# Kernel optimization log

Measured on AMD Instinct MI355X. Metric: run time of the kernel, lower is better.

## Reference

```python
import jax, jax.numpy as jnp
import numpy as np

B, H, S, D = 2, 16, 2048, 64

def setup_inputs() -> dict:
    key = jax.random.key(0)
    kq, kk, kv = jax.random.split(key, 3)
    Q = jax.random.normal(kq, (B, H, S, D), dtype=jnp.float32)
    K = jax.random.normal(kk, (B, H, S, D), dtype=jnp.float32)
    V = jax.random.normal(kv, (B, H, S, D), dtype=jnp.float32)
    d_sqrt = jnp.float32(np.sqrt(D))  # 8.0
    return {"Q": Q, "K": K, "V": V, "d_sqrt": d_sqrt}

def reference(Q, K, V, d_sqrt):
    # scores = Q @ K^T / d_sqrt  -> softmax over last axis -> @ V
    scores = jnp.einsum("bhqd,bhkd->bhqk", Q, K) / d_sqrt  # [B,H,S,S]
    attention = jax.nn.softmax(scores, axis=-1)
    return jnp.einsum("bhqk,bhkd->bhqd", attention, V)
```

## Files before the change

kernel.cpp:

```cpp
#include <hip/hip_runtime.h>
#include <hip/hip_bf16.h>


#define S_LEN 2048
#define DHEAD 64
#define QB 128
#define KB 64
#define NT (S_LEN / KB)
#define LDK 72

typedef __attribute__((ext_vector_type(8))) short short8;
typedef __attribute__((ext_vector_type(4))) short short4v;
typedef __attribute__((ext_vector_type(4))) float f32x4;

__device__ __forceinline__ unsigned pk2(float a, float b) {
  unsigned r;
  asm("v_cvt_pk_bf16_f32 %0, %1, %2" : "=v"(r) : "v"(a), "v"(b));
  return r;
}

#if __has_builtin(__builtin_amdgcn_exp2f)
#define EXP2(x) __builtin_amdgcn_exp2f(x)
#else
__device__ __forceinline__ float exp2_asm(float x) {
  float r; asm("v_exp_f32 %0, %1" : "=v"(r) : "v"(x)); return r;
}
#define EXP2(x) exp2_asm(x)
#endif

__device__ __forceinline__ f32x4 mfma16(short4v a, short4v b, f32x4 c) {
#if __has_builtin(__builtin_amdgcn_mfma_f32_16x16x16bf16_1k)
  return __builtin_amdgcn_mfma_f32_16x16x16bf16_1k(a, b, c, 0, 0, 0);
#else
  asm volatile("s_nop 1\n\t"
               "v_mfma_f32_16x16x16_bf16 %0, %1, %2, %0\n\t"
               "s_nop 7"
               : "+v"(c) : "v"(a), "v"(b));
  return c;
#endif
}

union frag8 { short8 s; unsigned u[4]; };
union frag4 { short4v s4; unsigned u[2]; };
union vpair { short8 s8; short4v h[2]; };

__global__ __launch_bounds__(512, 4) void attn_fwd_kernel(
    const float* __restrict__ Q, const float* __restrict__ K,
    const float* __restrict__ V, const float* __restrict__ dscale,
    float* __restrict__ O) {
  const int bx = blockIdx.x;
  const int qt = bx & 15;
  const int bh = bx >> 4;
  const float scale = 1.4426950408889634f / dscale[0];

  __shared__ unsigned short Klds[2][KB][LDK];
  __shared__ unsigned short Vtlds[2][DHEAD][LDK];

  const int tid = threadIdx.x;
  const int wid = tid >> 6;
  const int lane = tid & 63;
  const int lhi = lane >> 4;
  const int llo = lane & 15;

  const float* Qb = Q + (size_t)bh * S_LEN * DHEAD;
  const float* Kb = K + (size_t)bh * S_LEN * DHEAD;
  const float* Vb = V + (size_t)bh * S_LEN * DHEAD;
  float* Ob = O + (size_t)bh * S_LEN * DHEAD;

  frag8 qf0, qf1;
  {
    const int qrow = qt * QB + wid * 16 + llo;
    const float* qp = Qb + (size_t)qrow * DHEAD + lhi * 8;
    float4 a = *(const float4*)(qp);
    float4 b = *(const float4*)(qp + 4);
    float4 c = *(const float4*)(qp + 32);
    float4 d = *(const float4*)(qp + 36);
    qf0.u[0] = pk2(a.x * scale, a.y * scale);
    qf0.u[1] = pk2(a.z * scale, a.w * scale);
    qf0.u[2] = pk2(b.x * scale, b.y * scale);
    qf0.u[3] = pk2(b.z * scale, b.w * scale);
    qf1.u[0] = pk2(c.x * scale, c.y * scale);
    qf1.u[1] = pk2(c.z * scale, c.w * scale);
    qf1.u[2] = pk2(d.x * scale, d.y * scale);
    qf1.u[3] = pk2(d.z * scale, d.w * scale);
  }

  frag4 ones;
  ones.u[0] = 0x3f803f80u;
  ones.u[1] = 0x3f803f80u;

  f32x4 o[4], ol;
#pragma unroll
  for (int t = 0; t < 4; ++t) o[t] = (f32x4)0.0f;
  ol = (f32x4)0.0f;

  const int kr = tid >> 3;
  const int kc = (tid & 7) * 8;
  const int vd = tid & 63;
  const int vg0 = (wid >> 2) * 32 + (wid & 3) * 4;

  float4 ka, kb2;
  float va[8];
  {
    const float* kp = Kb + (size_t)(0 * KB + kr) * DHEAD + kc;
    ka = *(const float4*)kp;
    kb2 = *(const float4*)(kp + 4);
    const float* vp0 = Vb + (size_t)(0 * KB + vg0) * DHEAD + vd;
#pragma unroll
    for (int j = 0; j < 4; ++j) va[j] = vp0[j * DHEAD];
#pragma unroll
    for (int j = 0; j < 4; ++j) va[4 + j] = vp0[(16 + j) * DHEAD];
  }

  for (int kt = 0; kt < NT; ++kt) {
    const int cb = kt & 1;
    {
      uint4 kw;
      kw.x = pk2(ka.x, ka.y); kw.y = pk2(ka.z, ka.w);
      kw.z = pk2(kb2.x, kb2.y); kw.w = pk2(kb2.z, kb2.w);
      *(uint4*)&Klds[cb][kr][kc] = kw;
      uint4 vw;
      vw.x = pk2(va[0], va[1]); vw.y = pk2(va[2], va[3]);
      vw.z = pk2(va[4], va[5]); vw.w = pk2(va[6], va[7]);
      *(uint4*)&Vtlds[cb][vd][wid * 8] = vw;
    }
    __syncthreads();

    {
      const int nk = (kt + 1 < NT) ? kt + 1 : 0;
      const float* kp = Kb + (size_t)(nk * KB + kr) * DHEAD + kc;
      ka = *(const float4*)kp;
      kb2 = *(const float4*)(kp + 4);
      const float* vp0 = Vb + (size_t)(nk * KB + vg0) * DHEAD + vd;
#pragma unroll
      for (int j = 0; j < 4; ++j) va[j] = vp0[j * DHEAD];
#pragma unroll
      for (int j = 0; j < 4; ++j) va[4 + j] = vp0[(16 + j) * DHEAD];
    }

    f32x4 s[4];
    __builtin_amdgcn_s_setprio(1);
#pragma unroll
    for (int t = 0; t < 4; ++t) {
      short8 kf0 = *(const short8*)&Klds[cb][t * 16 + llo][lhi * 8];
      short8 kf1 = *(const short8*)&Klds[cb][t * 16 + llo][32 + lhi * 8];
      f32x4 acc = (f32x4)0.0f;
      acc = __builtin_amdgcn_mfma_f32_16x16x32_bf16(kf0, qf0.s, acc, 0, 0, 0);
      acc = __builtin_amdgcn_mfma_f32_16x16x32_bf16(kf1, qf1.s, acc, 0, 0, 0);
      s[t] = acc;
    }
    __builtin_amdgcn_s_setprio(0);

    frag4 pf[4];
#pragma unroll
    for (int t = 0; t < 4; ++t) {
      float p0 = EXP2(s[t][0]);
      float p1 = EXP2(s[t][1]);
      float p2 = EXP2(s[t][2]);
      float p3 = EXP2(s[t][3]);
      pf[t].u[0] = pk2(p0, p1);
      pf[t].u[1] = pk2(p2, p3);
    }

    __builtin_amdgcn_s_setprio(1);
#pragma unroll
    for (int dt = 0; dt < 4; ++dt) {
#pragma unroll
      for (int pr = 0; pr < 2; ++pr) {
        vpair vv;
        vv.s8 = *(const short8*)&Vtlds[cb][dt * 16 + llo][pr * 32 + lhi * 8];
        o[dt] = mfma16(vv.h[0], pf[2 * pr].s4, o[dt]);
        o[dt] = mfma16(vv.h[1], pf[2 * pr + 1].s4, o[dt]);
      }
    }
#pragma unroll
    for (int k16 = 0; k16 < 4; ++k16)
      ol = mfma16(ones.s4, pf[k16].s4, ol);
    __builtin_amdgcn_s_setprio(0);
  }

  const float inv = 1.0f / ol[0];
  const int qrow = qt * QB + wid * 16 + llo;
  float* op = Ob + (size_t)qrow * DHEAD;
#pragma unroll
  for (int dt = 0; dt < 4; ++dt) {
    float4 st;
    st.x = o[dt][0] * inv;
    st.y = o[dt][1] * inv;
    st.z = o[dt][2] * inv;
    st.w = o[dt][3] * inv;
    *(float4*)(op + dt * 16 + lhi * 4) = st;
  }
}

extern "C" void kernel_launch(void* const* d_in, const int* in_sizes, int n_in,
                              void* d_out, int out_size, void* d_ws, size_t ws_size,
                              hipStream_t stream) {
  const float* Q = (const float*)d_in[0];
  const float* K = (const float*)d_in[1];
  const float* V = (const float*)d_in[2];
  const float* dsq = (const float*)d_in[3];
  float* O = (float*)d_out;

  const int blocks = (2 * 16) * (S_LEN / QB);
  hipLaunchKernelGGL(attn_fwd_kernel, dim3(blocks), dim3(512), 0, stream,
                     Q, K, V, dsq, O);
}
```

Baseline: 132.9 us.

## Replace ones-MFMA row sum with VALU sum and interleave exp with PV MFMAs

New measurement: 134.0 us. Within noise of the previous version (+0.9%).

```diff
diff --git a/kernel.cpp b/kernel.cpp
--- a/kernel.cpp
+++ b/kernel.cpp
@@ -85,14 +85,10 @@
     qf1.u[3] = pk2(d.z * scale, d.w * scale);
   }
 
-  frag4 ones;
-  ones.u[0] = 0x3f803f80u;
-  ones.u[1] = 0x3f803f80u;
-
-  f32x4 o[4], ol;
+  f32x4 o[4];
 #pragma unroll
   for (int t = 0; t < 4; ++t) o[t] = (f32x4)0.0f;
-  ol = (f32x4)0.0f;
+  float lsum = 0.0f;
 
   const int kr = tid >> 3;
   const int kc = (tid & 7) * 8;
@@ -138,48 +134,77 @@
       for (int j = 0; j < 4; ++j) va[4 + j] = vp0[(16 + j) * DHEAD];
     }
 
+    short8 kf[8];
+#pragma unroll
+    for (int t = 0; t < 4; ++t) {
+      kf[2 * t] = *(const short8*)&Klds[cb][t * 16 + llo][lhi * 8];
+      kf[2 * t + 1] = *(const short8*)&Klds[cb][t * 16 + llo][32 + lhi * 8];
+    }
     f32x4 s[4];
     __builtin_amdgcn_s_setprio(1);
 #pragma unroll
     for (int t = 0; t < 4; ++t) {
-      short8 kf0 = *(const short8*)&Klds[cb][t * 16 + llo][lhi * 8];
-      short8 kf1 = *(const short8*)&Klds[cb][t * 16 + llo][32 + lhi * 8];
       f32x4 acc = (f32x4)0.0f;
-      acc = __builtin_amdgcn_mfma_f32_16x16x32_bf16(kf0, qf0.s, acc, 0, 0, 0);
-      acc = __builtin_amdgcn_mfma_f32_16x16x32_bf16(kf1, qf1.s, acc, 0, 0, 0);
+      acc = __builtin_amdgcn_mfma_f32_16x16x32_bf16(kf[2 * t], qf0.s, acc, 0, 0, 0);
+      acc = __builtin_amdgcn_mfma_f32_16x16x32_bf16(kf[2 * t + 1], qf1.s, acc, 0, 0, 0);
       s[t] = acc;
     }
     __builtin_amdgcn_s_setprio(0);
 
     frag4 pf[4];
-#pragma unroll
-    for (int t = 0; t < 4; ++t) {
+    float ls0 = 0.0f, ls1 = 0.0f;
+#pragma unroll
+    for (int t = 0; t < 2; ++t) {
       float p0 = EXP2(s[t][0]);
       float p1 = EXP2(s[t][1]);
       float p2 = EXP2(s[t][2]);
       float p3 = EXP2(s[t][3]);
       pf[t].u[0] = pk2(p0, p1);
       pf[t].u[1] = pk2(p2, p3);
+      ls0 += (p0 + p1) + (p2 + p3);
     }
 
     __builtin_amdgcn_s_setprio(1);
+    vpair vv0[4];
+#pragma unroll
+    for (int dt = 0; dt < 4; ++dt)
+      vv0[dt].s8 = *(const short8*)&Vtlds[cb][dt * 16 + llo][lhi * 8];
 #pragma unroll
     for (int dt = 0; dt < 4; ++dt) {
-#pragma unroll
-      for (int pr = 0; pr < 2; ++pr) {
-        vpair vv;
-        vv.s8 = *(const short8*)&Vtlds[cb][dt * 16 + llo][pr * 32 + lhi * 8];
-        o[dt] = mfma16(vv.h[0], pf[2 * pr].s4, o[dt]);
-        o[dt] = mfma16(vv.h[1], pf[2 * pr + 1].s4, o[dt]);
-      }
-    }
-#pragma unroll
-    for (int k16 = 0; k16 < 4; ++k16)
-      ol = mfma16(ones.s4, pf[k16].s4, ol);
+      o[dt] = mfma16(vv0[dt].h[0], pf[0].s4, o[dt]);
+      o[dt] = mfma16(vv0[dt].h[1], pf[1].s4, o[dt]);
+    }
     __builtin_amdgcn_s_setprio(0);
-  }
-
-  const float inv = 1.0f / ol[0];
+
+#pragma unroll
+    for (int t = 2; t < 4; ++t) {
+      float p0 = EXP2(s[t][0]);
+      float p1 = EXP2(s[t][1]);
+      float p2 = EXP2(s[t][2]);
+      float p3 = EXP2(s[t][3]);
+      pf[t].u[0] = pk2(p0, p1);
+      pf[t].u[1] = pk2(p2, p3);
+      ls1 += (p0 + p1) + (p2 + p3);
+    }
+    lsum += ls0 + ls1;
+
+    __builtin_amdgcn_s_setprio(1);
+    vpair vv1[4];
+#pragma unroll
+    for (int dt = 0; dt < 4; ++dt)
+      vv1[dt].s8 = *(const short8*)&Vtlds[cb][dt * 16 + llo][32 + lhi * 8];
+#pragma unroll
+    for (int dt = 0; dt < 4; ++dt) {
+      o[dt] = mfma16(vv1[dt].h[0], pf[2].s4, o[dt]);
+      o[dt] = mfma16(vv1[dt].h[1], pf[3].s4, o[dt]);
+    }
+    __builtin_amdgcn_s_setprio(0);
+  }
+
+  float l = lsum;
+  l += __shfl_xor(l, 16);
+  l += __shfl_xor(l, 32);
+  const float inv = 1.0f / l;
   const int qrow = qt * QB + wid * 16 + llo;
   float* op = Ob + (size_t)qrow * DHEAD;
 #pragma unroll
```
